# Optimization experiments

Measured on AMD Instinct MI355X. Metric: run time of the kernel, lower is better.

## Reference

```python
import jax, jax.numpy as jnp
import numpy as np

TAU = 1.0  # temperature of the tanh-Gumbel relaxation


def setup_inputs() -> dict:
    key = jax.random.key(0)
    k1, k2, k3 = jax.random.split(key, 3)
    B, C, F, W, H, K, S = 64, 256, 512, 64, 64, 3, 1
    x = jax.random.normal(k1, (B, C, W, H), dtype=jnp.float32)
    weight = jax.random.normal(k2, (F, C, K, K), dtype=jnp.float32) * 0.05
    # torch samples Uniform(1e-10, 1) fresh every forward; we make it an input
    epsilon = jax.random.uniform(k3, (S, F, C, K, K), dtype=jnp.float32,
                                 minval=1e-10, maxval=1.0)
    return {"x": x, "weight": weight, "epsilon": epsilon}


def reference(x, weight, epsilon):
    # delta: logistic noise; relaxed_weights = tanh((w + delta)/tau)
    delta = 0.5 * jnp.log(epsilon / (1.0 - epsilon))          # [s,f,c,k,l]
    relaxed_weights = jnp.tanh((weight + delta) / TAU)        # broadcast over s
    x5 = x[None]                                              # [1,b,c,w,h]
    # sums over kernel dims k,l (independent of x) and contracts channel c
    out = jnp.einsum('sfckl,sbcwh->sbfwh', relaxed_weights, x5)
    return out
```

## Files before the change

### kernel.cpp

```cpp
#include <hip/hip_runtime.h>
#include <hip/hip_bf16.h>
#include <stdint.h>

#define C_DIM 256
#define F_DIM 512
#define B_DIM 64
#define N_DIM 4096
#define BM 128
#define BN 128
#define BK 32
#define SB_STRIDE 80

typedef __bf16  bf16x8 __attribute__((ext_vector_type(8)));
typedef float   f32x4  __attribute__((ext_vector_type(4)));

__global__ void prep_w2(const float* __restrict__ w, const float* __restrict__ eps,
                        __hip_bfloat16* __restrict__ w2) {
    int id = blockIdx.x * blockDim.x + threadIdx.x;
    if (id >= F_DIM * C_DIM) return;
    const float* wp = w  + id * 9;
    const float* ep = eps + id * 9;
    float s = 0.f;
#pragma unroll
    for (int i = 0; i < 9; ++i) {
        float wi = wp[i], e = ep[i];
        float r = e / (1.0f - e);
        float t = __expf(2.0f * wi) * r;
        s += 1.0f - 2.0f / (t + 1.0f);
    }
    w2[id] = __float2bfloat16(s);
}

__device__ inline void load_lds16(const void* g, void* l) {
    __builtin_amdgcn_global_load_lds(
        (const __attribute__((address_space(1))) uint32_t*)g,
        (__attribute__((address_space(3))) uint32_t*)l, 16, 0, 0);
}

__device__ inline uint32_t pack_bf16x2(float a, float b) {
    union { __hip_bfloat162 h; uint32_t u; } c;
    c.h.x = __float2bfloat16(a);
    c.h.y = __float2bfloat16(b);
    return c.u;
}

__global__ __launch_bounds__(256)
void gemm_kernel(const float* __restrict__ X,
                 const __hip_bfloat16* __restrict__ W2,
                 float* __restrict__ Out) {
    __shared__ __hip_bfloat16 sA[BM * BK];
    __shared__ unsigned char  sB[BN * SB_STRIDE];

    const int tid  = threadIdx.x;
    const int lane = tid & 63;
    const int wave = tid >> 6;

    int wid  = (blockIdx.x & 7) * 1024 + (blockIdx.x >> 3);
    int fi   = wid & 3;
    int rest = wid >> 2;
    int ni   = rest & 31;
    int bi   = rest >> 5;

    const float* Xb           = X  + (size_t)bi * C_DIM * N_DIM + ni * BN;
    const __hip_bfloat16* Ab  = W2 + fi * BM * C_DIM;
    float* Ob                 = Out + ((size_t)bi * F_DIM + (size_t)fi * BM) * N_DIM + ni * BN;

    const int bn  = tid & 127;
    const int bkh = tid >> 7;

    f32x4 acc[4][4];
#pragma unroll
    for (int i = 0; i < 4; ++i)
#pragma unroll
        for (int j = 0; j < 4; ++j)
            acc[i][j] = (f32x4){0.f, 0.f, 0.f, 0.f};

    const int wm = (wave >> 1) * 64;
    const int wn = (wave & 1) * 64;
    const int l15 = lane & 15;
    const int l4  = lane >> 4;

    for (int kt = 0; kt < C_DIM; kt += BK) {
        __syncthreads();

#pragma unroll
        for (int j = 0; j < 2; ++j) {
            int slot = j * 256 + tid;
            int m  = slot >> 2;
            int k8 = slot & 3;
            const __hip_bfloat16* gp = Ab + m * C_DIM + kt + k8 * 8;
            char* lp = (char*)sA + (j * 256 + wave * 64) * 16;
            load_lds16((const void*)gp, (void*)lp);
        }

        float xv[4][4];
#pragma unroll
        for (int i = 0; i < 4; ++i) {
            int q  = bkh + 2 * i;
            const float* xp = Xb + (size_t)(kt + 4 * q) * N_DIM + bn;
#pragma unroll
            for (int d = 0; d < 4; ++d) xv[i][d] = xp[(size_t)d * N_DIM];
        }
#pragma unroll
        for (int i = 0; i < 4; ++i) {
            int q = bkh + 2 * i;
            uint2 v;
            v.x = pack_bf16x2(xv[i][0], xv[i][1]);
            v.y = pack_bf16x2(xv[i][2], xv[i][3]);
            *(uint2*)(&sB[bn * SB_STRIDE + q * 8]) = v;
        }

        __syncthreads();

        bf16x8 af[4], bfrag[4];
#pragma unroll
        for (int mi = 0; mi < 4; ++mi) {
            int m = wm + mi * 16 + l15;
            af[mi] = *(const bf16x8*)((const char*)sA + m * 64 + l4 * 16);
        }
#pragma unroll
        for (int nj = 0; nj < 4; ++nj) {
            int n = wn + nj * 16 + l15;
            bfrag[nj] = *(const bf16x8*)(&sB[n * SB_STRIDE + l4 * 16]);
        }
#pragma unroll
        for (int mi = 0; mi < 4; ++mi)
#pragma unroll
            for (int nj = 0; nj < 4; ++nj)
                acc[mi][nj] = __builtin_amdgcn_mfma_f32_16x16x32_bf16(
                    af[mi], bfrag[nj], acc[mi][nj], 0, 0, 0);
    }

#pragma unroll
    for (int mi = 0; mi < 4; ++mi) {
        int mrow = wm + mi * 16 + l4 * 4;
#pragma unroll
        for (int nj = 0; nj < 4; ++nj) {
            int ncol = wn + nj * 16 + l15;
            float* op = Ob + (size_t)mrow * N_DIM + ncol;
#pragma unroll
            for (int r = 0; r < 4; ++r)
                op[(size_t)r * N_DIM] = acc[mi][nj][r];
        }
    }
}

extern "C" void kernel_launch(void* const* d_in, const int* in_sizes, int n_in,
                              void* d_out, int out_size, void* d_ws, size_t ws_size,
                              hipStream_t stream) {
    const float* x   = (const float*)d_in[0];
    const float* w   = (const float*)d_in[1];
    const float* eps = (const float*)d_in[2];
    float* out       = (float*)d_out;
    __hip_bfloat16* w2 = (__hip_bfloat16*)d_ws;

    prep_w2<<<dim3((F_DIM * C_DIM + 255) / 256), dim3(256), 0, stream>>>(w, eps, w2);
    gemm_kernel<<<dim3(8192), dim3(256), 0, stream>>>(x, w2, out);
}
```

Measured before the change: 804.0 us.

## Stage full X column tile in LDS once and loop over all F tiles

Each block now converts its 256x128 slice of X to bf16 once, keeps it in swizzled LDS, and iterates over all four 128-row F tiles, streaming the small weight matrix in 64-wide K chunks. Previously each X tile was reloaded and reconverted from global memory by four separate blocks (one per F tile). The kernel uses 512-thread blocks, XOR swizzles on both LDS buffers to avoid bank conflicts, and nontemporal loads and stores. The tradeoffs are a larger LDS footprint (about 80KB per block), fewer blocks in the grid (2048), and a serial X-staging prologue with no overlap.

```diff
diff --git a/kernel.cpp b/kernel.cpp
--- a/kernel.cpp
+++ b/kernel.cpp
@@ -6,10 +6,10 @@
 #define F_DIM 512
 #define B_DIM 64
 #define N_DIM 4096
-#define BM 128
 #define BN 128
-#define BK 32
-#define SB_STRIDE 80
+#define BF 128
+#define BK 64
+#define NSTEP 16
 
 typedef __bf16  bf16x8 __attribute__((ext_vector_type(8)));
 typedef float   f32x4  __attribute__((ext_vector_type(4)));
@@ -44,103 +44,117 @@
     return c.u;
 }
 
-__global__ __launch_bounds__(256)
+__global__ __launch_bounds__(512, 4)
 void gemm_kernel(const float* __restrict__ X,
                  const __hip_bfloat16* __restrict__ W2,
                  float* __restrict__ Out) {
-    __shared__ __hip_bfloat16 sA[BM * BK];
-    __shared__ unsigned char  sB[BN * SB_STRIDE];
+    __shared__ unsigned char sX[BN * 512];
+    __shared__ unsigned char sA[BF * BK * 2];
 
     const int tid  = threadIdx.x;
     const int lane = tid & 63;
     const int wave = tid >> 6;
+    const int l15  = lane & 15;
+    const int l4   = lane >> 4;
 
-    int wid  = (blockIdx.x & 7) * 1024 + (blockIdx.x >> 3);
-    int fi   = wid & 3;
-    int rest = wid >> 2;
-    int ni   = rest & 31;
-    int bi   = rest >> 5;
+    const int bi = blockIdx.x >> 5;
+    const int ni = blockIdx.x & 31;
 
-    const float* Xb           = X  + (size_t)bi * C_DIM * N_DIM + ni * BN;
-    const __hip_bfloat16* Ab  = W2 + fi * BM * C_DIM;
-    float* Ob                 = Out + ((size_t)bi * F_DIM + (size_t)fi * BM) * N_DIM + ni * BN;
+    const float* Xb = X   + (size_t)bi * C_DIM * N_DIM + ni * BN;
+    float*       Ob = Out + (size_t)bi * F_DIM * N_DIM + ni * BN;
 
-    const int bn  = tid & 127;
-    const int bkh = tid >> 7;
+    {
+        const int n  = tid & 127;
+        const int ch = tid >> 7;
+        unsigned char* base = sX + n * 512;
+        const int sw = (n & 31) << 4;
+        const float* xp = Xb + n;
+#pragma unroll
+        for (int g = 0; g < 8; ++g) {
+            const int c0 = ch * 64 + g * 8;
+            float v[8];
+#pragma unroll
+            for (int r = 0; r < 8; ++r)
+                v[r] = __builtin_nontemporal_load(xp + (size_t)(c0 + r) * N_DIM);
+            uint4 pk;
+            pk.x = pack_bf16x2(v[0], v[1]);
+            pk.y = pack_bf16x2(v[2], v[3]);
+            pk.z = pack_bf16x2(v[4], v[5]);
+            pk.w = pack_bf16x2(v[6], v[7]);
+            *(uint4*)(base + ((c0 * 2) ^ sw)) = pk;
+        }
+    }
 
-    f32x4 acc[4][4];
+    const int wm = (wave >> 1) * 32;
+    const int wn = (wave & 1) * 64;
+
+    f32x4 acc[2][4];
 #pragma unroll
-    for (int i = 0; i < 4; ++i)
+    for (int mi = 0; mi < 2; ++mi)
 #pragma unroll
-        for (int j = 0; j < 4; ++j)
-            acc[i][j] = (f32x4){0.f, 0.f, 0.f, 0.f};
+        for (int nj = 0; nj < 4; ++nj)
+            acc[mi][nj] = (f32x4){0.f, 0.f, 0.f, 0.f};
 
-    const int wm = (wave >> 1) * 64;
-    const int wn = (wave & 1) * 64;
-    const int l15 = lane & 15;
-    const int l4  = lane >> 4;
+    for (int step = 0; step < NSTEP; ++step) {
+        const int ft = step >> 2;
+        const int kt = (step & 3) * BK;
 
-    for (int kt = 0; kt < C_DIM; kt += BK) {
         __syncthreads();
 
+        {
+            const __hip_bfloat16* Aft = W2 + (size_t)ft * BF * C_DIM + kt;
 #pragma unroll
-        for (int j = 0; j < 2; ++j) {
-            int slot = j * 256 + tid;
-            int m  = slot >> 2;
-            int k8 = slot & 3;
-            const __hip_bfloat16* gp = Ab + m * C_DIM + kt + k8 * 8;
-            char* lp = (char*)sA + (j * 256 + wave * 64) * 16;
-            load_lds16((const void*)gp, (void*)lp);
-        }
-
-        float xv[4][4];
-#pragma unroll
-        for (int i = 0; i < 4; ++i) {
-            int q  = bkh + 2 * i;
-            const float* xp = Xb + (size_t)(kt + 4 * q) * N_DIM + bn;
-#pragma unroll
-            for (int d = 0; d < 4; ++d) xv[i][d] = xp[(size_t)d * N_DIM];
-        }
-#pragma unroll
-        for (int i = 0; i < 4; ++i) {
-            int q = bkh + 2 * i;
-            uint2 v;
-            v.x = pack_bf16x2(xv[i][0], xv[i][1]);
-            v.y = pack_bf16x2(xv[i][2], xv[i][3]);
-            *(uint2*)(&sB[bn * SB_STRIDE + q * 8]) = v;
+            for (int j = 0; j < 2; ++j) {
+                int s = j * 512 + tid;
+                int m = s >> 3, g = s & 7;
+                const __hip_bfloat16* gp = Aft + m * C_DIM + ((g ^ (m & 7)) * 8);
+                char* lp = (char*)sA + (j * 512 + wave * 64) * 16;
+                load_lds16((const void*)gp, (void*)lp);
+            }
         }
 
         __syncthreads();
 
-        bf16x8 af[4], bfrag[4];
+        bf16x8 af[2][2], bfr[2][4];
 #pragma unroll
-        for (int mi = 0; mi < 4; ++mi) {
-            int m = wm + mi * 16 + l15;
-            af[mi] = *(const bf16x8*)((const char*)sA + m * 64 + l4 * 16);
+        for (int kk = 0; kk < 2; ++kk) {
+#pragma unroll
+            for (int mi = 0; mi < 2; ++mi) {
+                int m   = wm + mi * 16 + l15;
+                int col = (kk * 64 + l4 * 16) ^ ((m & 7) << 4);
+                af[kk][mi] = *(const bf16x8*)(sA + m * 128 + col);
+            }
+#pragma unroll
+            for (int nj = 0; nj < 4; ++nj) {
+                int n   = wn + nj * 16 + l15;
+                int col = (kt * 2 + kk * 64 + l4 * 16) ^ ((n & 31) << 4);
+                bfr[kk][nj] = *(const bf16x8*)(sX + n * 512 + col);
+            }
         }
 #pragma unroll
-        for (int nj = 0; nj < 4; ++nj) {
-            int n = wn + nj * 16 + l15;
-            bfrag[nj] = *(const bf16x8*)(&sB[n * SB_STRIDE + l4 * 16]);
-        }
+        for (int kk = 0; kk < 2; ++kk)
 #pragma unroll
-        for (int mi = 0; mi < 4; ++mi)
+            for (int mi = 0; mi < 2; ++mi)
 #pragma unroll
-            for (int nj = 0; nj < 4; ++nj)
-                acc[mi][nj] = __builtin_amdgcn_mfma_f32_16x16x32_bf16(
-                    af[mi], bfrag[nj], acc[mi][nj], 0, 0, 0);
-    }
+                for (int nj = 0; nj < 4; ++nj)
+                    acc[mi][nj] = __builtin_amdgcn_mfma_f32_16x16x32_bf16(
+                        af[kk][mi], bfr[kk][nj], acc[mi][nj], 0, 0, 0);
 
+        if ((step & 3) == 3) {
+            float* Oft = Ob + (size_t)(ft * BF) * N_DIM;
 #pragma unroll
-    for (int mi = 0; mi < 4; ++mi) {
-        int mrow = wm + mi * 16 + l4 * 4;
+            for (int mi = 0; mi < 2; ++mi) {
+                int mrow = wm + mi * 16 + l4 * 4;
 #pragma unroll
-        for (int nj = 0; nj < 4; ++nj) {
-            int ncol = wn + nj * 16 + l15;
-            float* op = Ob + (size_t)mrow * N_DIM + ncol;
+                for (int nj = 0; nj < 4; ++nj) {
+                    int ncol = wn + nj * 16 + l15;
+                    float* op = Oft + (size_t)mrow * N_DIM + ncol;
 #pragma unroll
-            for (int r = 0; r < 4; ++r)
-                op[(size_t)r * N_DIM] = acc[mi][nj][r];
+                    for (int r = 0; r < 4; ++r)
+                        __builtin_nontemporal_store(acc[mi][nj][r], op + (size_t)r * N_DIM);
+                    acc[mi][nj] = (f32x4){0.f, 0.f, 0.f, 0.f};
+                }
+            }
         }
     }
 }
@@ -155,5 +169,5 @@
     __hip_bfloat16* w2 = (__hip_bfloat16*)d_ws;
 
     prep_w2<<<dim3((F_DIM * C_DIM + 255) / 256), dim3(256), 0, stream>>>(w, eps, w2);
-    gemm_kernel<<<dim3(8192), dim3(256), 0, stream>>>(x, w2, out);
+    gemm_kernel<<<dim3(B_DIM * 32), dim3(512), 0, stream>>>(x, w2, out);
 }
```

Result: faster. 745.7 us (-7.3%).
